# Kernel optimization log

Measured on AMD Instinct MI355X. Metric: run time of the kernel, lower is better.

The kernel has to match this reference:

```python
import jax, jax.numpy as jnp
import numpy as np
from jax import lax

B, NS, SL, NF = 1024, 9, 36, 7
H, DM, DH, FFN = 2, 128, 64, 2048
EPS = 1e-5


def setup_inputs():
    ks = jax.random.split(jax.random.key(0), 12)
    r = lambda i, shape, s=0.05: jax.random.normal(ks[i], shape, dtype=jnp.float32) * s
    return {
        "x": jax.random.normal(ks[0], (B, NS, SL, NF), dtype=jnp.float32),
        "W_g1": r(1, (NS, 64)), "b_g1": jnp.zeros((64,), jnp.float32),
        "W_g2": r(2, (64, DM)), "b_g2": jnp.zeros((DM,), jnp.float32),
        "conv1_w": r(3, (64, NF, 5)), "conv1_b": jnp.zeros((64,), jnp.float32),
        "conv2_w": r(4, (DM, 64, 3)), "conv2_b": jnp.zeros((DM,), jnp.float32),
        "bn_g": jnp.ones((DM,), jnp.float32), "bn_b": jnp.zeros((DM,), jnp.float32),
        "bn_m": jnp.zeros((DM,), jnp.float32), "bn_v": jnp.ones((DM,), jnp.float32),
        "in_proj_w": r(5, (2, 3 * DM, DM)), "in_proj_b": jnp.zeros((2, 3 * DM), jnp.float32),
        "out_proj_w": r(6, (2, DM, DM)), "out_proj_b": jnp.zeros((2, DM), jnp.float32),
        "ln1_g": jnp.ones((2, DM), jnp.float32), "ln1_b": jnp.zeros((2, DM), jnp.float32),
        "ln2_g": jnp.ones((2, DM), jnp.float32), "ln2_b": jnp.zeros((2, DM), jnp.float32),
        "ffn_w1": r(7, (2, FFN, DM)), "ffn_b1": jnp.zeros((2, FFN), jnp.float32),
        "ffn_w2": r(8, (2, DM, FFN)), "ffn_b2": jnp.zeros((2, DM), jnp.float32),
        "attn_w": r(9, (DM, 1)), "attn_b": jnp.zeros((1,), jnp.float32),
        "fc_w": r(10, (DM, 1)), "fc_b": jnp.zeros((1,), jnp.float32),
    }


def _ln(z, g, b):
    m = jnp.mean(z, -1, keepdims=True)
    v = jnp.mean(jnp.square(z - m), -1, keepdims=True)
    return (z - m) * lax.rsqrt(v + EPS) * g + b


def _gcn_agg(h):
    # Fully-connected 9-node graph (softmax(adj) > 0 everywhere, incl. self loops):
    # GCN norm deg=9 -> rows 0..8 become the mean of rows 0..8.
    # Remaining rows only receive the add_remaining_self_loops self loop (deg=1) -> identity.
    return h.at[:NS].set(jnp.mean(h[:NS], axis=0, keepdims=True))


def _forward(x, W_g1, b_g1, W_g2, b_g2, conv1_w, conv1_b, conv2_w, conv2_b,
             bn_g, bn_b, bn_m, bn_v, in_proj_w, in_proj_b, out_proj_w, out_proj_b,
             ln1_g, ln1_b, ln2_g, ln2_b, ffn_w1, ffn_b1, ffn_w2, ffn_b2,
             attn_w, attn_b, fc_w, fc_b):
    Bx = x.shape[0]
    # ---- GCN branch (edge weights from softmax(adj) are never used by GCNConv) ----
    xg = jnp.mean(x, axis=-1).reshape(Bx * SL, NS)                 # (B*36, 9)
    h = jax.nn.relu(_gcn_agg(xg @ W_g1) + b_g1)                    # (B*36, 64)
    h = jax.nn.relu(_gcn_agg(h @ W_g2) + b_g2)                     # (B*36, 128)
    x_gcn = h.reshape(Bx, SL, DM)
    # ---- conv branch ----
    xc = x.reshape(Bx * NS, NF, SL)
    dn = ("NCH", "OIH", "NCH")
    c = lax.conv_general_dilated(xc, conv1_w, (1,), [(2, 2)], dimension_numbers=dn) + conv1_b[:, None]
    c = lax.conv_general_dilated(c, conv2_w, (1,), [(1, 1)], dimension_numbers=dn) + conv2_b[:, None]
    c = (c - bn_m[:, None]) * lax.rsqrt(bn_v[:, None] + EPS) * bn_g[:, None] + bn_b[:, None]
    # AdaptiveAvgPool1d(36) on length-36 input is identity; eval-mode dropout is identity.
    s = c.reshape(Bx, NS, DM, SL).mean(axis=1).transpose(0, 2, 1)  # (B, 36, 128) batch-first
    # ---- post-LN transformer encoder (torch defaults, eval mode) ----
    scale = 1.0 / np.sqrt(DH).astype(np.float32)
    for i in range(2):
        qkv = s @ in_proj_w[i].T + in_proj_b[i]                    # (B, 36, 384)
        q, k, v = jnp.split(qkv, 3, axis=-1)
        q = q.reshape(Bx, SL, H, DH).transpose(0, 2, 1, 3)
        k = k.reshape(Bx, SL, H, DH).transpose(0, 2, 1, 3)
        v = v.reshape(Bx, SL, H, DH).transpose(0, 2, 1, 3)
        a = jax.nn.softmax(jnp.einsum("bhqd,bhkd->bhqk", q, k) * scale, axis=-1)
        o = jnp.einsum("bhqk,bhkd->bhqd", a, v).transpose(0, 2, 1, 3).reshape(Bx, SL, DM)
        o = o @ out_proj_w[i].T + out_proj_b[i]
        s = _ln(s + o, ln1_g[i], ln1_b[i])
        f = jax.nn.relu(s @ ffn_w1[i].T + ffn_b1[i]) @ ffn_w2[i].T + ffn_b2[i]
        s = _ln(s + f, ln2_g[i], ln2_b[i])
    # ---- fuse branches + attention pooling + head ----
    s = s + x_gcn
    aw = jax.nn.softmax(s @ attn_w + attn_b, axis=1)               # softmax over seq dim
    pooled = jnp.sum(s * aw, axis=1)                               # (B, 128)
    out = pooled @ fc_w + fc_b                                     # (B, 1)
    return jnp.where(out >= 0, out, 0.1 * out)                     # LeakyReLU(0.1)


def reference(x, W_g1, b_g1, W_g2, b_g2, conv1_w, conv1_b, conv2_w, conv2_b,
              bn_g, bn_b, bn_m, bn_v, in_proj_w, in_proj_b, out_proj_w, out_proj_b,
              ln1_g, ln1_b, ln2_g, ln2_b, ffn_w1, ffn_b1, ffn_w2, ffn_b2,
              attn_w, attn_b, fc_w, fc_b):
    return _forward(x, W_g1, b_g1, W_g2, b_g2, conv1_w, conv1_b, conv2_w, conv2_b,
                    bn_g, bn_b, bn_m, bn_v, in_proj_w, in_proj_b, out_proj_w, out_proj_b,
                    ln1_g, ln1_b, ln2_g, ln2_b, ffn_w1, ffn_b1, ffn_w2, ffn_b2,
                    attn_w, attn_b, fc_w, fc_b)
```

## Files before the change

kernel.cpp:

```cpp
#include <hip/hip_runtime.h>
#include <math.h>

#define EPSV   1e-5f

typedef __attribute__((ext_vector_type(8))) short bf16x8;
typedef __attribute__((ext_vector_type(4))) float f32x4;

__device__ __forceinline__ short f2bf(float f){
    unsigned u = __float_as_uint(f);
    u += 0x7fffu + ((u >> 16) & 1u);
    return (short)(u >> 16);
}
__device__ __forceinline__ f32x4 mfma16(bf16x8 a, bf16x8 b, f32x4 c){
    return __builtin_amdgcn_mfma_f32_16x16x32_bf16(a, b, c, 0, 0, 0);
}
__device__ __forceinline__ bf16x8 ldfrag(const short* base, int row, int kbyte, int rowBytes){
    int byte = row * rowBytes + kbyte;
    byte ^= (row & 7) << 4;
    return *(const bf16x8*)((const char*)base + byte);
}
__device__ __forceinline__ bf16x8 ldfragG(const short* base, int row, int kbyte, int rowBytes){
    return *(const bf16x8*)((const char*)base + (size_t)row * rowBytes + kbyte);
}
__device__ __forceinline__ void stswz(short* base, int row, int col, int rowBytes, short v){
    int byte = row * rowBytes + col * 2;
    byte ^= (row & 7) << 4;
    *(short*)((char*)base + byte) = v;
}

__global__ __launch_bounds__(256) void cvt_all(
    const float* __restrict__ ipw, const float* __restrict__ opw,
    const float* __restrict__ fw1, const float* __restrict__ fw2,
    short* __restrict__ dst)
{
    int i = (blockIdx.x * 256 + threadIdx.x) * 4;
    if (i >= 1179648) return;
    const float* src; int off;
    if (i < 98304)       { src = ipw; off = i; }
    else if (i < 131072) { src = opw; off = i - 98304; }
    else if (i < 655360) { src = fw1; off = i - 131072; }
    else {
        int o  = i - 655360;
        int L  = o >> 18;
        int oo = o & 262143;
        int s0 = oo & 7;
        int lg = (oo >> 3) & 3;
        int c  = (oo >> 5) & 127;
        int grp = oo >> 12;
        int n  = grp * 32 + ((s0 >> 2) << 4) + lg * 4;
        src = fw2; off = L * 262144 + c * 2048 + n;
        float4 v = *(const float4*)(src + off);
        short4 s;
        s.x = f2bf(v.x); s.y = f2bf(v.y); s.z = f2bf(v.z); s.w = f2bf(v.w);
        *(short4*)(dst + i) = s;
        return;
    }
    float4 v = *(const float4*)(src + off);
    short4 s;
    s.x = f2bf(v.x); s.y = f2bf(v.y); s.z = f2bf(v.z); s.w = f2bf(v.w);
    *(short4*)(dst + i) = s;
}

__global__ __launch_bounds__(256) void gcn_all(
    const float* __restrict__ x,
    const float* __restrict__ Wg1, const float* __restrict__ bg1,
    const float* __restrict__ Wg2, const float* __restrict__ bg2,
    float* __restrict__ xgcn)
{
    int tid = threadIdx.x;
    if (blockIdx.x == 18432) {
        __shared__ float xgm[9];
        __shared__ float h1s[64];
        if (tid < 9) {
            float s = 0.f;
            for (int r = 0; r < 9; ++r) {
                const float* xp = x + (r * 9 + tid) * 7;
                #pragma unroll
                for (int f = 0; f < 7; ++f) s += xp[f];
            }
            xgm[tid] = s * (1.f / 63.f);
        }
        __syncthreads();
        if (tid < 64) {
            float acc = bg1[tid];
            #pragma unroll
            for (int j = 0; j < 9; ++j) acc += xgm[j] * Wg1[j * 64 + tid];
            h1s[tid] = fmaxf(acc, 0.f);
        }
        __syncthreads();
        if (tid < 128) {
            float acc = bg2[tid];
            #pragma unroll 8
            for (int c = 0; c < 64; ++c) acc += h1s[c] * Wg2[c * 128 + tid];
            float v = fmaxf(acc, 0.f);
            for (int r = 0; r < 9; ++r) xgcn[r * 128 + tid] = v;
        }
        return;
    }

    __shared__ float xg[2][9];
    __shared__ float h1[2][64];
    int ri = tid >> 7;
    int tr = tid & 127;
    int row = blockIdx.x * 2 + ri;

    if (tr < 9) {
        const float* xp = x + (row * 9 + tr) * 7;
        float s = 0.f;
        #pragma unroll
        for (int f = 0; f < 7; ++f) s += xp[f];
        xg[ri][tr] = s * (1.f / 7.f);
    }
    __syncthreads();
    if (tr < 64) {
        float acc = bg1[tr];
        #pragma unroll
        for (int j = 0; j < 9; ++j) acc += xg[ri][j] * Wg1[j * 64 + tr];
        h1[ri][tr] = fmaxf(acc, 0.f);
    }
    __syncthreads();
    if (row >= 9) {
        float acc = bg2[tr];
        #pragma unroll 8
        for (int c = 0; c < 64; ++c) acc += h1[ri][c] * Wg2[c * 128 + tr];
        xgcn[row * 128 + tr] = fmaxf(acc, 0.f);
    }
}

__global__ __launch_bounds__(256) void conv_branch(
    const float* __restrict__ x,
    const float* __restrict__ w1, const float* __restrict__ cb1,
    const float* __restrict__ w2, const float* __restrict__ cb2,
    const float* __restrict__ bng, const float* __restrict__ bnb,
    const float* __restrict__ bnm, const float* __restrict__ bnv,
    float* __restrict__ sbuf)
{
    __shared__ float xm[7 * 40];
    __shared__ float w1s[64 * 35];
    __shared__ float o1[64 * 38];
    int tid = threadIdx.x;
    int b = blockIdx.x;

    for (int idx = tid; idx < 7 * 40; idx += 256) xm[idx] = 0.f;
    for (int idx = tid; idx < 64 * 38; idx += 256) o1[idx] = 0.f;
    for (int idx = tid; idx < 2240; idx += 256) w1s[idx] = w1[idx];
    __syncthreads();

    const float* xb = x + (size_t)b * 2268;
    for (int idx = tid; idx < 252; idx += 256) {
        int f = idx / 36, l = idx - f * 36;
        float s = 0.f;
        #pragma unroll
        for (int n = 0; n < 9; ++n) s += xb[n * 252 + idx];
        xm[f * 40 + l + 2] = s * (1.f / 9.f);
    }
    __syncthreads();

    {
        int o = tid & 63, lh = tid >> 6;
        int l0 = lh * 9;
        float acc[9];
        float bias = cb1[o];
        #pragma unroll
        for (int r = 0; r < 9; ++r) acc[r] = bias;
        #pragma unroll
        for (int i = 0; i < 7; ++i) {
            #pragma unroll
            for (int k = 0; k < 5; ++k) {
                float w = w1s[o * 35 + i * 5 + k];
                const float* xrow = &xm[i * 40 + l0 + k];
                #pragma unroll
                for (int r = 0; r < 9; ++r) acc[r] += w * xrow[r];
            }
        }
        #pragma unroll
        for (int r = 0; r < 9; ++r) o1[o * 38 + l0 + r + 1] = acc[r];
    }
    __syncthreads();

    {
        int c = tid & 127, lh = tid >> 7;
        int l0 = lh * 18;
        float acc[18];
        #pragma unroll
        for (int r = 0; r < 18; ++r) acc[r] = 0.f;
        const float* w2c = w2 + c * 192;
        for (int i = 0; i < 64; ++i) {
            float wa = w2c[i * 3 + 0], wb = w2c[i * 3 + 1], wc = w2c[i * 3 + 2];
            const float* orow = &o1[i * 38 + l0];
            #pragma unroll
            for (int r = 0; r < 18; ++r)
                acc[r] += wa * orow[r] + wb * orow[r + 1] + wc * orow[r + 2];
        }
        float scale = bng[c] * rsqrtf(bnv[c] + EPSV);
        float shift = bnb[c] - bnm[c] * scale;
        float bias  = cb2[c];
        float* sb = sbuf + ((size_t)b * 36 + l0) * 128 + c;
        #pragma unroll
        for (int r = 0; r < 18; ++r)
            sb[r * 128] = (acc[r] + bias) * scale + shift;
    }
}

__global__ __launch_bounds__(256, 2) void attn_mfma(
    float* __restrict__ sbuf,
    const short* __restrict__ ipwb, const float* __restrict__ ipb,
    const short* __restrict__ opwb, const float* __restrict__ opb,
    const float* __restrict__ l1g, const float* __restrict__ l1b)
{
    __shared__ short Sb[48 * 128] __attribute__((aligned(16)));
    __shared__ char  U[38912]     __attribute__((aligned(16)));
    __shared__ float scf[36 * 40];
    short* Qb = (short*)U;
    short* Kb = (short*)(U + 6144);
    short* Vt = (short*)(U + 12288);
    short* Pb = (short*)(U + 20480);
    short* Hb = (short*)(U + 26624);

    const int tid  = threadIdx.x;
    const int wid  = tid >> 6;
    const int lane = tid & 63;
    const int lr   = lane & 15;
    const int lg   = lane >> 4;
    const int kbse = lg * 16;

    float* sg = sbuf + (size_t)blockIdx.x * 4608;
    const f32x4 fzero = {0.f, 0.f, 0.f, 0.f};

    for (int idx = tid; idx < 4608; idx += 256) {
        int r = idx >> 7, c = idx & 127;
        stswz(Sb, r, c, 256, f2bf(sg[idx]));
    }
    for (int idx = tid; idx < 1024; idx += 256)
        stswz(Vt, idx >> 4, 48 + (idx & 15), 128, 0);
    __syncthreads();

    for (int h = 0; h < 2; ++h) {
        {
            f32x4 acc[3][3];
            #pragma unroll
            for (int a = 0; a < 3; ++a)
                #pragma unroll
                for (int m = 0; m < 3; ++m) acc[a][m] = fzero;
            const int wrow0 = h * 64 + wid * 16 + lr;
            #pragma unroll
            for (int ks = 0; ks < 4; ++ks) {
                bf16x8 a0 = ldfrag(Sb,      lr, ks * 64 + kbse, 256);
                bf16x8 a1 = ldfrag(Sb, 16 + lr, ks * 64 + kbse, 256);
                bf16x8 a2 = ldfrag(Sb, 32 + lr, ks * 64 + kbse, 256);
                #pragma unroll
                for (int mat = 0; mat < 3; ++mat) {
                    bf16x8 bf = ldfragG(ipwb, mat * 128 + wrow0, ks * 64 + kbse, 256);
                    acc[mat][0] = mfma16(a0, bf, acc[mat][0]);
                    acc[mat][1] = mfma16(a1, bf, acc[mat][1]);
                    acc[mat][2] = mfma16(a2, bf, acc[mat][2]);
                }
            }
            int col = wid * 16 + lr;
            #pragma unroll
            for (int mat = 0; mat < 3; ++mat) {
                float bias = ipb[mat * 128 + h * 64 + col];
                #pragma unroll
                for (int mt = 0; mt < 3; ++mt) {
                    f32x4 c4 = acc[mat][mt];
                    if (mat == 0) {
                        #pragma unroll
                        for (int j = 0; j < 4; ++j)
                            stswz(Qb, mt * 16 + lg * 4 + j, col, 128, f2bf(c4[j] + bias));
                    } else if (mat == 1) {
                        #pragma unroll
                        for (int j = 0; j < 4; ++j)
                            stswz(Kb, mt * 16 + lg * 4 + j, col, 128, f2bf(c4[j] + bias));
                    } else {
                        int rbase = mt * 16 + lg * 4;
                        short4 s4;
                        s4.x = f2bf(rbase + 0 < 36 ? c4[0] + bias : 0.f);
                        s4.y = f2bf(rbase + 1 < 36 ? c4[1] + bias : 0.f);
                        s4.z = f2bf(rbase + 2 < 36 ? c4[2] + bias : 0.f);
                        s4.w = f2bf(rbase + 3 < 36 ? c4[3] + bias : 0.f);
                        int byte = col * 128 + rbase * 2;
                        byte ^= (col & 7) << 4;
                        *(short4*)((char*)Vt + byte) = s4;
                    }
                }
            }
        }
        __syncthreads();

        for (int t = wid; t < 9; t += 4) {
            int mt = t / 3, nt = t - mt * 3;
            f32x4 acc = fzero;
            #pragma unroll
            for (int ks = 0; ks < 2; ++ks) {
                bf16x8 a = ldfrag(Qb, mt * 16 + lr, ks * 64 + kbse, 128);
                bf16x8 b = ldfrag(Kb, nt * 16 + lr, ks * 64 + kbse, 128);
                acc = mfma16(a, b, acc);
            }
            int col = nt * 16 + lr;
            if (col < 36) {
                #pragma unroll
                for (int j = 0; j < 4; ++j) {
                    int r = mt * 16 + lg * 4 + j;
                    if (r < 36) scf[r * 40 + col] = acc[j] * 0.125f;
                }
            }
        }
        __syncthreads();

        {
            int g = tid >> 2, e = tid & 3;
            if (g < 36) {
                float v[9];
                float mx = -1e30f;
                #pragma unroll
                for (int i = 0; i < 9; ++i) { v[i] = scf[g * 40 + e * 9 + i]; mx = fmaxf(mx, v[i]); }
                mx = fmaxf(mx, __shfl_xor(mx, 1));
                mx = fmaxf(mx, __shfl_xor(mx, 2));
                float ssum = 0.f;
                #pragma unroll
                for (int i = 0; i < 9; ++i) { v[i] = __expf(v[i] - mx); ssum += v[i]; }
                ssum += __shfl_xor(ssum, 1);
                ssum += __shfl_xor(ssum, 2);
                float inv = 1.f / ssum;
                #pragma unroll
                for (int i = 0; i < 9; ++i)
                    stswz(Pb, g, e * 9 + i, 128, f2bf(v[i] * inv));
                #pragma unroll
                for (int i = 0; i < 7; ++i)
                    stswz(Pb, g, 36 + e * 7 + i, 128, 0);
            }
        }
        __syncthreads();

        {
            f32x4 oacc[3] = {fzero, fzero, fzero};
            #pragma unroll
            for (int ks = 0; ks < 2; ++ks) {
                bf16x8 b = ldfrag(Vt, wid * 16 + lr, ks * 64 + kbse, 128);
                #pragma unroll
                for (int mt = 0; mt < 3; ++mt) {
                    bf16x8 a = ldfrag(Pb, mt * 16 + lr, ks * 64 + kbse, 128);
                    oacc[mt] = mfma16(a, b, oacc[mt]);
                }
            }
            int col = h * 64 + wid * 16 + lr;
            #pragma unroll
            for (int mt = 0; mt < 3; ++mt)
                #pragma unroll
                for (int j = 0; j < 4; ++j)
                    stswz(Hb, mt * 16 + lg * 4 + j, col, 256, f2bf(oacc[mt][j]));
        }
        __syncthreads();
    }

    float z[3][2][4];
    {
        f32x4 pacc[3][2];
        #pragma unroll
        for (int m = 0; m < 3; ++m) { pacc[m][0] = fzero; pacc[m][1] = fzero; }
        #pragma unroll
        for (int ks = 0; ks < 4; ++ks) {
            bf16x8 a0 = ldfrag(Hb,      lr, ks * 64 + kbse, 256);
            bf16x8 a1 = ldfrag(Hb, 16 + lr, ks * 64 + kbse, 256);
            bf16x8 a2 = ldfrag(Hb, 32 + lr, ks * 64 + kbse, 256);
            #pragma unroll
            for (int t = 0; t < 2; ++t) {
                bf16x8 b = ldfragG(opwb, (wid * 2 + t) * 16 + lr, ks * 64 + kbse, 256);
                pacc[0][t] = mfma16(a0, b, pacc[0][t]);
                pacc[1][t] = mfma16(a1, b, pacc[1][t]);
                pacc[2][t] = mfma16(a2, b, pacc[2][t]);
            }
        }
        #pragma unroll
        for (int t = 0; t < 2; ++t) {
            int col = (wid * 2 + t) * 16 + lr;
            float bias = opb[col];
            #pragma unroll
            for (int mt = 0; mt < 3; ++mt)
                #pragma unroll
                for (int j = 0; j < 4; ++j) {
                    int r = mt * 16 + lg * 4 + j;
                    z[mt][t][j] = (r < 36) ? pacc[mt][t][j] + bias + sg[r * 128 + col] : 0.f;
                }
        }
    }
    {
        float* part = scf;
        #pragma unroll
        for (int mt = 0; mt < 3; ++mt)
            #pragma unroll
            for (int j = 0; j < 4; ++j) {
                int r = mt * 16 + lg * 4 + j;
                float s  = z[mt][0][j] + z[mt][1][j];
                float ss = z[mt][0][j] * z[mt][0][j] + z[mt][1][j] * z[mt][1][j];
                s  += __shfl_xor(s, 1);  s  += __shfl_xor(s, 2);
                s  += __shfl_xor(s, 4);  s  += __shfl_xor(s, 8);
                ss += __shfl_xor(ss, 1); ss += __shfl_xor(ss, 2);
                ss += __shfl_xor(ss, 4); ss += __shfl_xor(ss, 8);
                if (lr == 0 && r < 36) { part[r * 8 + wid] = s; part[r * 8 + 4 + wid] = ss; }
            }
    }
    __syncthreads();
    {
        const float* part = scf;
        #pragma unroll
        for (int mt = 0; mt < 3; ++mt)
            #pragma unroll
            for (int j = 0; j < 4; ++j) {
                int r = mt * 16 + lg * 4 + j;
                if (r < 36) {
                    float s  = part[r * 8 + 0] + part[r * 8 + 1] + part[r * 8 + 2] + part[r * 8 + 3];
                    float ss = part[r * 8 + 4] + part[r * 8 + 5] + part[r * 8 + 6] + part[r * 8 + 7];
                    float mean = s * (1.f / 128.f);
                    float rstd = rsqrtf(ss * (1.f / 128.f) - mean * mean + EPSV);
                    #pragma unroll
                    for (int t = 0; t < 2; ++t) {
                        int col = (wid * 2 + t) * 16 + lr;
                        float v = (z[mt][t][j] - mean) * rstd * l1g[col] + l1b[col];
                        sg[r * 128 + col] = v;
                    }
                }
            }
    }
}

__global__ __launch_bounds__(128, 1) void ffn_v4(
    float* __restrict__ sres,
    const short* __restrict__ fw1b, const float* __restrict__ fb1,
    const short* __restrict__ fw2p, const float* __restrict__ fb2,
    const float* __restrict__ l2g, const float* __restrict__ l2b)
{
    __shared__ short Wbuf[2][16384] __attribute__((aligned(16)));

    const int tid  = threadIdx.x;
    const int wid  = tid >> 6;
    const int lane = tid & 63;
    const int lr   = lane & 15;
    const int lg   = lane >> 4;
    const size_t row0 = (size_t)blockIdx.x * 64 + wid * 32;
    const f32x4 fzero = {0.f, 0.f, 0.f, 0.f};

    bf16x8 sfrag[2][4];
    #pragma unroll
    for (int rt = 0; rt < 2; ++rt) {
        const float* sp = sres + (row0 + rt * 16 + lr) * 128;
        #pragma unroll
        for (int ks = 0; ks < 4; ++ks) {
            float4 lo = *(const float4*)(sp + ks * 32 + lg * 8);
            float4 hi = *(const float4*)(sp + ks * 32 + lg * 8 + 4);
            bf16x8 f;
            f[0] = f2bf(lo.x); f[1] = f2bf(lo.y); f[2] = f2bf(lo.z); f[3] = f2bf(lo.w);
            f[4] = f2bf(hi.x); f[5] = f2bf(hi.y); f[6] = f2bf(hi.z); f[7] = f2bf(hi.w);
            sfrag[rt][ks] = f;
        }
    }

    f32x4 facc[2][8];
    #pragma unroll
    for (int rt = 0; rt < 2; ++rt)
        #pragma unroll
        for (int ct = 0; ct < 8; ++ct) facc[rt][ct] = fzero;

    bf16x8 g1[8], g2[8];
    #pragma unroll
    for (int i = 0; i < 8; ++i) {
        int fid = tid + 128 * i;
        g1[i] = *(const bf16x8*)((const char*)fw1b + fid * 16);
        g2[i] = *(const bf16x8*)((const char*)fw2p + fid * 16);
    }
    #pragma unroll
    for (int i = 0; i < 8; ++i) {
        int fid = tid + 128 * i;
        int swz = (fid * 16) ^ (((fid >> 4) & 7) << 4);
        *(bf16x8*)((char*)&Wbuf[0][0] + swz)         = g1[i];
        *(bf16x8*)((char*)&Wbuf[0][8192] + fid * 16) = g2[i];
    }

#define FFN_CHUNK(Q, CUR, NXT)                                                    \
    {                                                                             \
        const int q = (Q);                                                        \
        if (q < 31) {                                                             \
            const char* b1p = (const char*)fw1b + (q + 1) * 16384;                \
            const char* b2p = (const char*)fw2p + (q + 1) * 16384;                \
            _Pragma("unroll")                                                     \
            for (int i = 0; i < 8; ++i) {                                         \
                int fid = tid + 128 * i;                                          \
                g1[i] = *(const bf16x8*)(b1p + fid * 16);                         \
                g2[i] = *(const bf16x8*)(b2p + fid * 16);                         \
            }                                                                     \
        }                                                                         \
        __syncthreads();                 \
        const short* W1l = &Wbuf[CUR][0];                                         \
        const short* W2l = &Wbuf[CUR][8192];                                      \
              \
        f32x4 hacc[2][4];                                                         \
        _Pragma("unroll")                                                         \
        for (int rt = 0; rt < 2; ++rt)                                            \
            _Pragma("unroll")                                                     \
            for (int nt = 0; nt < 4; ++nt) hacc[rt][nt] = fzero;                  \
        _Pragma("unroll")                                                         \
        for (int ks = 0; ks < 4; ++ks)                                            \
            _Pragma("unroll")                                                     \
            for (int nt = 0; nt < 4; ++nt) {                                      \
                bf16x8 a = ldfrag(W1l, nt * 16 + lr, ks * 64 + lg * 16, 256);     \
                hacc[0][nt] = mfma16(a, sfrag[0][ks], hacc[0][nt]);               \
                hacc[1][nt] = mfma16(a, sfrag[1][ks], hacc[1][nt]);               \
            }                                                                     \
        \
        bf16x8 hf[2][2];                                                          \
        _Pragma("unroll")                                                         \
        for (int ksn = 0; ksn < 2; ++ksn) {                                       \
            float4 bA = *(const float4*)(fb1 + q * 64 + ksn * 32 + lg * 4);       \
            float4 bB = *(const float4*)(fb1 + q * 64 + ksn * 32 + 16 + lg * 4);  \
            _Pragma("unroll")                                                     \
            for (int rt = 0; rt < 2; ++rt) {                                      \
                bf16x8 h;                                                         \
                h[0] = f2bf(fmaxf(hacc[rt][ksn * 2][0]     + bA.x, 0.f));         \
                h[1] = f2bf(fmaxf(hacc[rt][ksn * 2][1]     + bA.y, 0.f));         \
                h[2] = f2bf(fmaxf(hacc[rt][ksn * 2][2]     + bA.z, 0.f));         \
                h[3] = f2bf(fmaxf(hacc[rt][ksn * 2][3]     + bA.w, 0.f));         \
                h[4] = f2bf(fmaxf(hacc[rt][ksn * 2 + 1][0] + bB.x, 0.f));         \
                h[5] = f2bf(fmaxf(hacc[rt][ksn * 2 + 1][1] + bB.y, 0.f));         \
                h[6] = f2bf(fmaxf(hacc[rt][ksn * 2 + 1][2] + bB.z, 0.f));         \
                h[7] = f2bf(fmaxf(hacc[rt][ksn * 2 + 1][3] + bB.w, 0.f));         \
                hf[rt][ksn] = h;                                                  \
            }                                                                     \
        }                                                                         \
                     \
        _Pragma("unroll")                                                         \
        for (int ksn = 0; ksn < 2; ++ksn)                                         \
            _Pragma("unroll")                                                     \
            for (int ct = 0; ct < 8; ++ct) {                                      \
                bf16x8 b2 = *(const bf16x8*)(W2l +                                \
                              ((ksn * 128 + ct * 16 + lr) * 4 + lg) * 8);         \
                facc[0][ct] = mfma16(hf[0][ksn], b2, facc[0][ct]);                \
                facc[1][ct] = mfma16(hf[1][ksn], b2, facc[1][ct]);                \
            }                                                                     \
        if (q < 31) {                                                             \
            char* d1 = (char*)&Wbuf[NXT][0];                                      \
            char* d2 = (char*)&Wbuf[NXT][8192];                                   \
            _Pragma("unroll")                                                     \
            for (int i = 0; i < 8; ++i) {                                         \
                int fid = tid + 128 * i;                                          \
                int swz = (fid * 16) ^ (((fid >> 4) & 7) << 4);                   \
                *(bf16x8*)(d1 + swz)        = g1[i];                              \
                *(bf16x8*)(d2 + fid * 16)   = g2[i];                              \
            }                                                                     \
        }                                                                         \
    }

    #pragma unroll 1
    for (int qq = 0; qq < 16; ++qq) {
        FFN_CHUNK(2 * qq,     0, 1)
        FFN_CHUNK(2 * qq + 1, 1, 0)
    }
#undef FFN_CHUNK

    #pragma unroll
    for (int rt = 0; rt < 2; ++rt) {
        const size_t rowb = row0 + rt * 16;
        float zv[8][4];
        #pragma unroll
        for (int ct = 0; ct < 8; ++ct) {
            int c = ct * 16 + lr;
            float b2v = fb2[c];
            #pragma unroll
            for (int j = 0; j < 4; ++j)
                zv[ct][j] = facc[rt][ct][j] + b2v + sres[(rowb + lg * 4 + j) * 128 + c];
        }
        #pragma unroll
        for (int j = 0; j < 4; ++j) {
            float s = 0.f, sq = 0.f;
            #pragma unroll
            for (int ct = 0; ct < 8; ++ct) { s += zv[ct][j]; sq += zv[ct][j] * zv[ct][j]; }
            s  += __shfl_xor(s, 1);  s  += __shfl_xor(s, 2);
            s  += __shfl_xor(s, 4);  s  += __shfl_xor(s, 8);
            sq += __shfl_xor(sq, 1); sq += __shfl_xor(sq, 2);
            sq += __shfl_xor(sq, 4); sq += __shfl_xor(sq, 8);
            float mean = s * (1.f / 128.f);
            float rstd = rsqrtf(sq * (1.f / 128.f) - mean * mean + EPSV);
            float* og = sres + (rowb + lg * 4 + j) * 128;
            #pragma unroll
            for (int ct = 0; ct < 8; ++ct) {
                int c = ct * 16 + lr;
                og[c] = (zv[ct][j] - mean) * rstd * l2g[c] + l2b[c];
            }
        }
    }
}

__global__ __launch_bounds__(128) void pool_head(
    const float* __restrict__ sbuf, const float* __restrict__ xgcn,
    const float* __restrict__ aww, const float* __restrict__ awb,
    const float* __restrict__ fcw, const float* __restrict__ fcb,
    float* __restrict__ out)
{
    __shared__ float sl[36][128];
    __shared__ float zz[36];
    __shared__ float p[128];
    int tid = threadIdx.x;
    int b = blockIdx.x;
    const float* sg = sbuf + (size_t)b * 4608;
    const float* gg = xgcn + (size_t)b * 4608;
    for (int idx = tid; idx < 4608; idx += 128)
        sl[0][idx] = sg[idx] + gg[idx];
    __syncthreads();
    if (tid < 36) {
        float acc = awb[0];
        #pragma unroll
        for (int j = 0; j < 128; j += 4) {
            float4 s4 = *(const float4*)&sl[tid][j];
            float4 w4 = *(const float4*)(aww + j);
            acc += s4.x * w4.x + s4.y * w4.y + s4.z * w4.z + s4.w * w4.w;
        }
        zz[tid] = acc;
    }
    __syncthreads();
    if (tid == 0) {
        float m = -1e30f;
        for (int k = 0; k < 36; ++k) m = fmaxf(m, zz[k]);
        float ssum = 0.f;
        for (int k = 0; k < 36; ++k) ssum += __expf(zz[k] - m);
        float inv = 1.f / ssum;
        for (int k = 0; k < 36; ++k) zz[k] = __expf(zz[k] - m) * inv;
    }
    __syncthreads();
    {
        float acc = 0.f;
        for (int l = 0; l < 36; ++l) acc += sl[l][tid] * zz[l];
        p[tid] = acc;
    }
    __syncthreads();
    if (tid == 0) {
        float acc = fcb[0];
        for (int dd = 0; dd < 128; ++dd) acc += p[dd] * fcw[dd];
        out[b] = acc >= 0.f ? acc : 0.1f * acc;
    }
}

extern "C" void kernel_launch(void* const* d_in, const int* in_sizes, int n_in,
                              void* d_out, int out_size, void* d_ws, size_t ws_size,
                              hipStream_t stream)
{
    const float* x   = (const float*)d_in[0];
    const float* Wg1 = (const float*)d_in[1];
    const float* bg1 = (const float*)d_in[2];
    const float* Wg2 = (const float*)d_in[3];
    const float* bg2 = (const float*)d_in[4];
    const float* c1w = (const float*)d_in[5];
    const float* c1b = (const float*)d_in[6];
    const float* c2w = (const float*)d_in[7];
    const float* c2b = (const float*)d_in[8];
    const float* bng = (const float*)d_in[9];
    const float* bnb = (const float*)d_in[10];
    const float* bnm = (const float*)d_in[11];
    const float* bnv = (const float*)d_in[12];
    const float* ipw = (const float*)d_in[13];
    const float* ipb = (const float*)d_in[14];
    const float* opw = (const float*)d_in[15];
    const float* opb = (const float*)d_in[16];
    const float* l1g = (const float*)d_in[17];
    const float* l1b = (const float*)d_in[18];
    const float* l2g = (const float*)d_in[19];
    const float* l2b = (const float*)d_in[20];
    const float* fw1 = (const float*)d_in[21];
    const float* fb1 = (const float*)d_in[22];
    const float* fw2 = (const float*)d_in[23];
    const float* fb2 = (const float*)d_in[24];
    const float* aww = (const float*)d_in[25];
    const float* awb = (const float*)d_in[26];
    const float* fcw = (const float*)d_in[27];
    const float* fcb = (const float*)d_in[28];
    float* out = (float*)d_out;

    float* sbuf = (float*)d_ws;
    float* xgcn = sbuf + (size_t)1024 * 36 * 128;
    short* wb   = (short*)(xgcn + (size_t)1024 * 36 * 128);
    short* ipwb = wb;
    short* opwb = wb + 98304;
    short* fw1b = wb + 131072;
    short* fw2p = wb + 655360;

    cvt_all<<<1152, 256, 0, stream>>>(ipw, opw, fw1, fw2, wb);
    gcn_all<<<18433, 256, 0, stream>>>(x, Wg1, bg1, Wg2, bg2, xgcn);
    conv_branch<<<1024, 256, 0, stream>>>(x, c1w, c1b, c2w, c2b,
                                          bng, bnb, bnm, bnv, sbuf);
    for (int i = 0; i < 2; ++i) {
        attn_mfma<<<1024, 256, 0, stream>>>(sbuf,
            ipwb + (size_t)i * 49152, ipb + (size_t)i * 384,
            opwb + (size_t)i * 16384, opb + (size_t)i * 128,
            l1g + (size_t)i * 128, l1b + (size_t)i * 128);
        ffn_v4<<<576, 128, 0, stream>>>(sbuf,
            fw1b + (size_t)i * 262144, fb1 + (size_t)i * 2048,
            fw2p + (size_t)i * 262144, fb2 + (size_t)i * 128,
            l2g + (size_t)i * 128, l2b + (size_t)i * 128);
    }
    pool_head<<<1024, 128, 0, stream>>>(sbuf, xgcn, aww, awb, fcw, fcb, out);
}
```

Measured before the change: 417.4 us.

## Restructure FFN kernel to four waves of 16 rows with 32-wide hidden chunks

The FFN kernel moves from 2 waves of 32 rows each to 4 waves of 16 rows each per block. The hidden dimension is now streamed in 64 chunks of 32 instead of 32 chunks of 64, which halves the LDS double-buffer and the per-thread accumulator and staging registers. Launch bounds allow 4 blocks per CU, aiming for more resident waves to hide global and LDS latency. In exchange, each weight tile in LDS is reused by fewer rows per wave, and the loop does twice as many barriers.

```diff
diff --git a/kernel.cpp b/kernel.cpp
--- a/kernel.cpp
+++ b/kernel.cpp
@@ -424,26 +424,25 @@
     }
 }
 
-__global__ __launch_bounds__(128, 1) void ffn_v4(
+__global__ __launch_bounds__(256, 4) void ffn_v5(
     float* __restrict__ sres,
     const short* __restrict__ fw1b, const float* __restrict__ fb1,
     const short* __restrict__ fw2p, const float* __restrict__ fb2,
     const float* __restrict__ l2g, const float* __restrict__ l2b)
 {
-    __shared__ short Wbuf[2][16384] __attribute__((aligned(16)));
+    __shared__ short Wbuf[2][8192] __attribute__((aligned(16)));
 
     const int tid  = threadIdx.x;
     const int wid  = tid >> 6;
     const int lane = tid & 63;
     const int lr   = lane & 15;
     const int lg   = lane >> 4;
-    const size_t row0 = (size_t)blockIdx.x * 64 + wid * 32;
+    const size_t row0 = (size_t)blockIdx.x * 64 + wid * 16;
     const f32x4 fzero = {0.f, 0.f, 0.f, 0.f};
 
-    bf16x8 sfrag[2][4];
-    #pragma unroll
-    for (int rt = 0; rt < 2; ++rt) {
-        const float* sp = sres + (row0 + rt * 16 + lr) * 128;
+    bf16x8 sfrag[4];
+    {
+        const float* sp = sres + (row0 + lr) * 128;
         #pragma unroll
         for (int ks = 0; ks < 4; ++ks) {
             float4 lo = *(const float4*)(sp + ks * 32 + lg * 8);
@@ -451,97 +450,79 @@
             bf16x8 f;
             f[0] = f2bf(lo.x); f[1] = f2bf(lo.y); f[2] = f2bf(lo.z); f[3] = f2bf(lo.w);
             f[4] = f2bf(hi.x); f[5] = f2bf(hi.y); f[6] = f2bf(hi.z); f[7] = f2bf(hi.w);
-            sfrag[rt][ks] = f;
-        }
-    }
-
-    f32x4 facc[2][8];
+            sfrag[ks] = f;
+        }
+    }
+
+    f32x4 facc[8];
     #pragma unroll
-    for (int rt = 0; rt < 2; ++rt)
-        #pragma unroll
-        for (int ct = 0; ct < 8; ++ct) facc[rt][ct] = fzero;
-
-    bf16x8 g1[8], g2[8];
+    for (int ct = 0; ct < 8; ++ct) facc[ct] = fzero;
+
+    bf16x8 g1[2], g2[2];
     #pragma unroll
-    for (int i = 0; i < 8; ++i) {
-        int fid = tid + 128 * i;
+    for (int i = 0; i < 2; ++i) {
+        int fid = tid + 256 * i;
         g1[i] = *(const bf16x8*)((const char*)fw1b + fid * 16);
         g2[i] = *(const bf16x8*)((const char*)fw2p + fid * 16);
     }
     #pragma unroll
-    for (int i = 0; i < 8; ++i) {
-        int fid = tid + 128 * i;
+    for (int i = 0; i < 2; ++i) {
+        int fid = tid + 256 * i;
         int swz = (fid * 16) ^ (((fid >> 4) & 7) << 4);
         *(bf16x8*)((char*)&Wbuf[0][0] + swz)         = g1[i];
-        *(bf16x8*)((char*)&Wbuf[0][8192] + fid * 16) = g2[i];
+        *(bf16x8*)((char*)&Wbuf[0][4096] + fid * 16) = g2[i];
     }
 
 #define FFN_CHUNK(Q, CUR, NXT)                                                    \
     {                                                                             \
         const int q = (Q);                                                        \
-        if (q < 31) {                                                             \
-            const char* b1p = (const char*)fw1b + (q + 1) * 16384;                \
-            const char* b2p = (const char*)fw2p + (q + 1) * 16384;                \
+        if (q < 63) {                                                             \
+            const char* b1p = (const char*)fw1b + (q + 1) * 8192;                 \
+            const char* b2p = (const char*)fw2p + (q + 1) * 8192;                 \
             _Pragma("unroll")                                                     \
-            for (int i = 0; i < 8; ++i) {                                         \
-                int fid = tid + 128 * i;                                          \
+            for (int i = 0; i < 2; ++i) {                                         \
+                int fid = tid + 256 * i;                                          \
                 g1[i] = *(const bf16x8*)(b1p + fid * 16);                         \
                 g2[i] = *(const bf16x8*)(b2p + fid * 16);                         \
             }                                                                     \
         }                                                                         \
         __syncthreads();                 \
         const short* W1l = &Wbuf[CUR][0];                                         \
-        const short* W2l = &Wbuf[CUR][8192];                                      \
-              \
-        f32x4 hacc[2][4];                                                         \
+        const short* W2l = &Wbuf[CUR][4096];                                      \
+                   \
+        f32x4 hacc[2];                                                            \
+        hacc[0] = fzero; hacc[1] = fzero;                                         \
         _Pragma("unroll")                                                         \
-        for (int rt = 0; rt < 2; ++rt)                                            \
+        for (int ks = 0; ks < 4; ++ks) {                                          \
+            bf16x8 a0 = ldfrag(W1l,      lr, ks * 64 + lg * 16, 256);             \
+            bf16x8 a1 = ldfrag(W1l, 16 + lr, ks * 64 + lg * 16, 256);             \
+            hacc[0] = mfma16(a0, sfrag[ks], hacc[0]);                             \
+            hacc[1] = mfma16(a1, sfrag[ks], hacc[1]);                             \
+        }                                                                         \
+                 \
+        float4 bA = *(const float4*)(fb1 + q * 32 + lg * 4);                      \
+        float4 bB = *(const float4*)(fb1 + q * 32 + 16 + lg * 4);                 \
+        bf16x8 hf;                                                                \
+        hf[0] = f2bf(fmaxf(hacc[0][0] + bA.x, 0.f));                              \
+        hf[1] = f2bf(fmaxf(hacc[0][1] + bA.y, 0.f));                              \
+        hf[2] = f2bf(fmaxf(hacc[0][2] + bA.z, 0.f));                              \
+        hf[3] = f2bf(fmaxf(hacc[0][3] + bA.w, 0.f));                              \
+        hf[4] = f2bf(fmaxf(hacc[1][0] + bB.x, 0.f));                              \
+        hf[5] = f2bf(fmaxf(hacc[1][1] + bB.y, 0.f));                              \
+        hf[6] = f2bf(fmaxf(hacc[1][2] + bB.z, 0.f));                              \
+        hf[7] = f2bf(fmaxf(hacc[1][3] + bB.w, 0.f));                              \
+         \
+        _Pragma("unroll")                                                         \
+        for (int ct = 0; ct < 8; ++ct) {                                          \
+            bf16x8 b2 = *(const bf16x8*)(W2l + ((ct * 16 + lr) * 4 + lg) * 8);    \
+            facc[ct] = mfma16(hf, b2, facc[ct]);                                  \
+        }                                                                         \
+        if (q < 63) {                                                             \
+            char* d1 = (char*)&Wbuf[NXT][0];                                      \
+            char* d2 = (char*)&Wbuf[NXT][4096];                                   \
             _Pragma("unroll")                                                     \
-            for (int nt = 0; nt < 4; ++nt) hacc[rt][nt] = fzero;                  \
-        _Pragma("unroll")                                                         \
-        for (int ks = 0; ks < 4; ++ks)                                            \
-            _Pragma("unroll")                                                     \
-            for (int nt = 0; nt < 4; ++nt) {                                      \
-                bf16x8 a = ldfrag(W1l, nt * 16 + lr, ks * 64 + lg * 16, 256);     \
-                hacc[0][nt] = mfma16(a, sfrag[0][ks], hacc[0][nt]);               \
-                hacc[1][nt] = mfma16(a, sfrag[1][ks], hacc[1][nt]);               \
-            }                                                                     \
-        \
-        bf16x8 hf[2][2];                                                          \
-        _Pragma("unroll")                                                         \
-        for (int ksn = 0; ksn < 2; ++ksn) {                                       \
-            float4 bA = *(const float4*)(fb1 + q * 64 + ksn * 32 + lg * 4);       \
-            float4 bB = *(const float4*)(fb1 + q * 64 + ksn * 32 + 16 + lg * 4);  \
-            _Pragma("unroll")                                                     \
-            for (int rt = 0; rt < 2; ++rt) {                                      \
-                bf16x8 h;                                                         \
-                h[0] = f2bf(fmaxf(hacc[rt][ksn * 2][0]     + bA.x, 0.f));         \
-                h[1] = f2bf(fmaxf(hacc[rt][ksn * 2][1]     + bA.y, 0.f));         \
-                h[2] = f2bf(fmaxf(hacc[rt][ksn * 2][2]     + bA.z, 0.f));         \
-                h[3] = f2bf(fmaxf(hacc[rt][ksn * 2][3]     + bA.w, 0.f));         \
-                h[4] = f2bf(fmaxf(hacc[rt][ksn * 2 + 1][0] + bB.x, 0.f));         \
-                h[5] = f2bf(fmaxf(hacc[rt][ksn * 2 + 1][1] + bB.y, 0.f));         \
-                h[6] = f2bf(fmaxf(hacc[rt][ksn * 2 + 1][2] + bB.z, 0.f));         \
-                h[7] = f2bf(fmaxf(hacc[rt][ksn * 2 + 1][3] + bB.w, 0.f));         \
-                hf[rt][ksn] = h;                                                  \
-            }                                                                     \
-        }                                                                         \
-                     \
-        _Pragma("unroll")                                                         \
-        for (int ksn = 0; ksn < 2; ++ksn)                                         \
-            _Pragma("unroll")                                                     \
-            for (int ct = 0; ct < 8; ++ct) {                                      \
-                bf16x8 b2 = *(const bf16x8*)(W2l +                                \
-                              ((ksn * 128 + ct * 16 + lr) * 4 + lg) * 8);         \
-                facc[0][ct] = mfma16(hf[0][ksn], b2, facc[0][ct]);                \
-                facc[1][ct] = mfma16(hf[1][ksn], b2, facc[1][ct]);                \
-            }                                                                     \
-        if (q < 31) {                                                             \
-            char* d1 = (char*)&Wbuf[NXT][0];                                      \
-            char* d2 = (char*)&Wbuf[NXT][8192];                                   \
-            _Pragma("unroll")                                                     \
-            for (int i = 0; i < 8; ++i) {                                         \
-                int fid = tid + 128 * i;                                          \
+            for (int i = 0; i < 2; ++i) {                                         \
+                int fid = tid + 256 * i;                                          \
                 int swz = (fid * 16) ^ (((fid >> 4) & 7) << 4);                   \
                 *(bf16x8*)(d1 + swz)        = g1[i];                              \
                 *(bf16x8*)(d2 + fid * 16)   = g2[i];                              \
@@ -550,41 +531,37 @@
     }
 
     #pragma unroll 1
-    for (int qq = 0; qq < 16; ++qq) {
+    for (int qq = 0; qq < 32; ++qq) {
         FFN_CHUNK(2 * qq,     0, 1)
         FFN_CHUNK(2 * qq + 1, 1, 0)
     }
 #undef FFN_CHUNK
 
+    float zv[8][4];
     #pragma unroll
-    for (int rt = 0; rt < 2; ++rt) {
-        const size_t rowb = row0 + rt * 16;
-        float zv[8][4];
+    for (int ct = 0; ct < 8; ++ct) {
+        int c = ct * 16 + lr;
+        float b2v = fb2[c];
+        #pragma unroll
+        for (int j = 0; j < 4; ++j)
+            zv[ct][j] = facc[ct][j] + b2v + sres[(row0 + lg * 4 + j) * 128 + c];
+    }
+    #pragma unroll
+    for (int j = 0; j < 4; ++j) {
+        float s = 0.f, sq = 0.f;
+        #pragma unroll
+        for (int ct = 0; ct < 8; ++ct) { s += zv[ct][j]; sq += zv[ct][j] * zv[ct][j]; }
+        s  += __shfl_xor(s, 1);  s  += __shfl_xor(s, 2);
+        s  += __shfl_xor(s, 4);  s  += __shfl_xor(s, 8);
+        sq += __shfl_xor(sq, 1); sq += __shfl_xor(sq, 2);
+        sq += __shfl_xor(sq, 4); sq += __shfl_xor(sq, 8);
+        float mean = s * (1.f / 128.f);
+        float rstd = rsqrtf(sq * (1.f / 128.f) - mean * mean + EPSV);
+        float* og = sres + (row0 + lg * 4 + j) * 128;
         #pragma unroll
         for (int ct = 0; ct < 8; ++ct) {
             int c = ct * 16 + lr;
-            float b2v = fb2[c];
-            #pragma unroll
-            for (int j = 0; j < 4; ++j)
-                zv[ct][j] = facc[rt][ct][j] + b2v + sres[(rowb + lg * 4 + j) * 128 + c];
-        }
-        #pragma unroll
-        for (int j = 0; j < 4; ++j) {
-            float s = 0.f, sq = 0.f;
-            #pragma unroll
-            for (int ct = 0; ct < 8; ++ct) { s += zv[ct][j]; sq += zv[ct][j] * zv[ct][j]; }
-            s  += __shfl_xor(s, 1);  s  += __shfl_xor(s, 2);
-            s  += __shfl_xor(s, 4);  s  += __shfl_xor(s, 8);
-            sq += __shfl_xor(sq, 1); sq += __shfl_xor(sq, 2);
-            sq += __shfl_xor(sq, 4); sq += __shfl_xor(sq, 8);
-            float mean = s * (1.f / 128.f);
-            float rstd = rsqrtf(sq * (1.f / 128.f) - mean * mean + EPSV);
-            float* og = sres + (rowb + lg * 4 + j) * 128;
-            #pragma unroll
-            for (int ct = 0; ct < 8; ++ct) {
-                int c = ct * 16 + lr;
-                og[c] = (zv[ct][j] - mean) * rstd * l2g[c] + l2b[c];
-            }
+            og[c] = (zv[ct][j] - mean) * rstd * l2g[c] + l2b[c];
         }
     }
 }
@@ -690,7 +667,7 @@
             ipwb + (size_t)i * 49152, ipb + (size_t)i * 384,
             opwb + (size_t)i * 16384, opb + (size_t)i * 128,
             l1g + (size_t)i * 128, l1b + (size_t)i * 128);
-        ffn_v4<<<576, 128, 0, stream>>>(sbuf,
+        ffn_v5<<<576, 256, 0, stream>>>(sbuf,
             fw1b + (size_t)i * 262144, fb1 + (size_t)i * 2048,
             fw2p + (size_t)i * 262144, fb2 + (size_t)i * 128,
             l2g + (size_t)i * 128, l2b + (size_t)i * 128);
```

After: 337.0 us. -19.3%, faster.
